# Optimization experiments

Measured on AMD Instinct MI355X. Metric: run time of the kernel, lower is better.

## Reference

```python
import jax, jax.numpy as jnp
import numpy as np

DR = 0.1
L = 24.0
N_FRAMES = 16
N_ATOMS = 512


def setup_inputs() -> dict:
    key = jax.random.key(0)
    # coordinates uniform in the periodic box [0, L)^3
    traj = jax.random.uniform(key, (N_FRAMES, N_ATOMS, 3), dtype=jnp.float32) * L
    cell = jnp.eye(3, dtype=jnp.float32) * L
    # r_list = arange(0.5*dr, L_max - 2*dr, dr) with L_max = cell[0,0]/2 -> 118 bins
    r_list = jnp.arange(0.5 * DR, L / 2 - 2 * DR, DR, dtype=jnp.float32)
    return {"traj": traj, "cell": cell, "r_list": r_list}


def _frame_hist(q, cell_diag, r_list, cutoff_sq):
    # q: [N,3]; dense minimum-image pairwise displacements, upper-triangle pairs only
    disp = q[None, :, :] - q[:, None, :]                        # [N,N,3]
    offsets = jax.lax.stop_gradient(jnp.floor(disp / cell_diag + 0.5))
    disp = disp - offsets * cell_diag                           # minimum image
    sq = jnp.sum(disp * disp, axis=-1)                          # [N,N]
    n = q.shape[0]
    triu = jnp.triu(jnp.ones((n, n), dtype=bool))               # torch.triu zeros lower part
    sq = jnp.where(triu, sq, 0.0)
    mask = (sq < cutoff_sq) & (sq != 0.0)                       # i<j and within cutoff
    d = jnp.sqrt(jnp.where(mask, sq, 1.0))                      # safe sqrt (masked out below)
    centered = d[:, :, None] - r_list[None, None, :]            # [N,N,B]
    g = (1.0 / (DR * np.sqrt(2.0 * np.pi))) * jnp.exp(-0.5 * (centered / DR) ** 2)
    g = g * mask[:, :, None].astype(g.dtype)                    # drop excluded pairs (== nonzero extraction)
    return g.sum(axis=(0, 1)) * DR                              # [B]


def reference(traj, cell, r_list):
    cell_diag = jnp.diag(cell)                                  # [3]
    cutoff_sq = (cell[0, 0] / 2.0) ** 2                         # L_max = cell[0,0]/2 (default)

    def step(acc, q):
        return acc + _frame_hist(q, cell_diag, r_list, cutoff_sq), None

    hist0 = jnp.zeros(r_list.shape, dtype=traj.dtype)
    hist, _ = jax.lax.scan(step, hist0, traj)                   # accumulate over frames like the python loop
    hist = hist / traj.shape[0]

    v = (4.0 * np.pi / 3.0) * ((r_list + 0.5 * DR) ** 3 - (r_list - 0.5 * DR) ** 3)
    natom = traj.shape[1]
    det = jnp.linalg.det(cell)
    gr = hist / v * det / (natom - 1) / natom * 2.0
    return (r_list, gr)
```

## Files before the change

kernel.cpp:

```cpp
#include <hip/hip_runtime.h>
#include <math.h>

#define N_ATOMS 512
#define MAX_B 128
#define NBUCK 128
#define WIN 0.40f

__global__ void zero_kernel(float* p, int n) {
    int t = blockIdx.x * blockDim.x + threadIdx.x;
    if (t < n) p[t] = 0.0f;
}

__global__ __launch_bounds__(256) void pair_kernel(
    const float* __restrict__ traj, const float* __restrict__ cell,
    const float* __restrict__ r_list, float* __restrict__ part,
    int B, int atomic_mode)
{
    __shared__ float2 qxy[N_ATOMS];
    __shared__ float  qzs[N_ATOMS];
    __shared__ float  dsorted[2048];
    __shared__ int    cnt[NBUCK];
    __shared__ int    start[NBUCK + 1];
    __shared__ int    cursor[NBUCK];
    __shared__ float  accbuf[256];

    const int frame = blockIdx.x >> 6;
    const int sub   = blockIdx.x & 63;
    const int tid   = threadIdx.x;

    const float* q = traj + (size_t)frame * (N_ATOMS * 3);
    for (int a = tid; a < N_ATOMS; a += 256) {
        qxy[a] = make_float2(q[3 * a + 0], q[3 * a + 1]);
        qzs[a] = q[3 * a + 2];
    }
    if (tid < NBUCK) cnt[tid] = 0;
    __syncthreads();

    const float L = cell[0];
    const float invL = 1.0f / L;
    const float cutoff_sq = 0.25f * L * L;
    const float inv_bw = (float)NBUCK / (0.5f * L);

    float dval[8];
    int   dbuck[8];
    #pragma unroll
    for (int s = 0; s < 8; ++s) {
        const int qidx = s * 256 + tid;
        const int rp   = sub * 4 + (qidx >> 9);
        const int qq   = qidx & 511;
        const int lenA = 511 - rp;
        const bool inA = qq < lenA;
        const int i = inA ? rp : (510 - rp);
        const int j = inA ? (rp + 1 + qq) : qq;
        const bool vp = !(rp == 255 && !inA);

        const float2 pj = qxy[j];
        const float2 pi = qxy[i];
        float dx = pj.x - pi.x;
        float dy = pj.y - pi.y;
        float dz = qzs[j] - qzs[i];
        dx -= L * floorf(dx * invL + 0.5f);
        dy -= L * floorf(dy * invL + 0.5f);
        dz -= L * floorf(dz * invL + 0.5f);
        const float d2 = dx * dx + dy * dy + dz * dz;

        dbuck[s] = -1;
        dval[s]  = 0.0f;
        if (vp && d2 < cutoff_sq && d2 != 0.0f) {
            const float d = sqrtf(d2);
            int b = (int)(d * inv_bw);
            if (b > NBUCK - 1) b = NBUCK - 1;
            dval[s]  = d;
            dbuck[s] = b;
            atomicAdd(&cnt[b], 1);
        }
    }
    __syncthreads();

    if (tid < 64) {
        const int c0 = cnt[2 * tid];
        const int c1 = cnt[2 * tid + 1];
        const int p  = c0 + c1;
        int incl = p;
        #pragma unroll
        for (int off = 1; off < 64; off <<= 1) {
            const int n = __shfl_up(incl, off, 64);
            if (tid >= off) incl += n;
        }
        start[2 * tid + 2]  = incl;
        start[2 * tid + 1]  = incl - c1;
        cursor[2 * tid]     = incl - p;
        cursor[2 * tid + 1] = incl - c1;
        if (tid == 0) start[0] = 0;
    }
    __syncthreads();

    #pragma unroll
    for (int s = 0; s < 8; ++s) {
        if (dbuck[s] >= 0) {
            const int pos = atomicAdd(&cursor[dbuck[s]], 1);
            dsorted[pos] = dval[s];
        }
    }
    __syncthreads();

    const int rot = (sub & 3) << 5;
    const int k = (tid + rot) & 127;
    const int g = tid >> 7;
    float acc = 0.0f;
    if (k < B) {
        const float rk = r_list[k];
        const float c1 = -50.0f;
        const float c2 = 100.0f * rk;
        const float c3 = -50.0f * rk * rk;
        int blo = (int)(fmaxf((rk - WIN) * inv_bw, 0.0f));
        int bhi = (int)((rk + WIN) * inv_bw);
        if (bhi > NBUCK - 1) bhi = NBUCK - 1;
        const int lo = start[blo];
        const int hi = start[bhi + 1];
        int idx = lo + g;
        int nn = hi - idx;
        nn = (nn > 0) ? ((nn + 1) >> 1) : 0;
        float acc1 = 0.0f;
        int m = nn >> 1;
        while (m-- > 0) {
            const float d0 = dsorted[idx];
            const float d1 = dsorted[idx + 2];
            idx += 4;
            acc  += __expf(fmaf(d0, fmaf(c1, d0, c2), c3));
            acc1 += __expf(fmaf(d1, fmaf(c1, d1, c2), c3));
        }
        if (nn & 1) {
            const float d0 = dsorted[idx];
            acc += __expf(fmaf(d0, fmaf(c1, d0, c2), c3));
        }
        acc += acc1;
    }
    accbuf[tid] = acc;
    __syncthreads();

    if (tid < 128) {
        const int kb = (tid + rot) & 127;
        const float v = accbuf[tid] + accbuf[tid + 128];
        if (atomic_mode) atomicAdd(&part[(blockIdx.x & 15) * MAX_B + kb], v);
        else             part[(size_t)blockIdx.x * MAX_B + kb] = v;
    }
}

__global__ __launch_bounds__(256) void finalize_kernel(
    const float* __restrict__ r_list, const float* __restrict__ cell,
    const float* __restrict__ part, float* __restrict__ out,
    int B, int F, int nrows)
{
    __shared__ float red[256];
    const int k = blockIdx.x;
    if (k >= B) return;

    float s = 0.0f;
    for (int t = threadIdx.x; t < nrows; t += 256) s += part[(size_t)t * MAX_B + k];
    red[threadIdx.x] = s;
    __syncthreads();
    for (int off = 128; off > 0; off >>= 1) {
        if (threadIdx.x < off) red[threadIdx.x] += red[threadIdx.x + off];
        __syncthreads();
    }
    if (threadIdx.x == 0) {
        const float r = r_list[k];
        out[k] = r;
        const float det = cell[0] * cell[4] * cell[8];
        const float rp = r + 0.05f;
        const float rm = r - 0.05f;
        const float v = (4.0f * (float)M_PI / 3.0f) * (rp * rp * rp - rm * rm * rm);
        const float inv_sqrt2pi = 0.3989422804014327f;
        const float h = red[0] * inv_sqrt2pi / (float)F;
        const float gr = h / v * det / (float)(N_ATOMS - 1) / (float)N_ATOMS * 2.0f;
        out[B + k] = gr;
    }
}

extern "C" void kernel_launch(void* const* d_in, const int* in_sizes, int n_in,
                              void* d_out, int out_size, void* d_ws, size_t ws_size,
                              hipStream_t stream) {
    const float* traj   = (const float*)d_in[0];
    const float* cell   = (const float*)d_in[1];
    const float* r_list = (const float*)d_in[2];
    float* out  = (float*)d_out;
    float* part = (float*)d_ws;

    const int B = in_sizes[2];
    const int F = in_sizes[0] / (N_ATOMS * 3);
    const int nblocks = F * 64;

    const bool partials_fit =
        ws_size >= (size_t)nblocks * MAX_B * sizeof(float);

    if (partials_fit) {
        hipLaunchKernelGGL(pair_kernel, dim3(nblocks), dim3(256), 0, stream,
                           traj, cell, r_list, part, B, 0);
        hipLaunchKernelGGL(finalize_kernel, dim3(MAX_B), dim3(256), 0, stream,
                           r_list, cell, part, out, B, F, nblocks);
    } else {
        hipLaunchKernelGGL(zero_kernel, dim3(8), dim3(256), 0, stream,
                           part, 16 * MAX_B);
        hipLaunchKernelGGL(pair_kernel, dim3(nblocks), dim3(256), 0, stream,
                           traj, cell, r_list, part, B, 1);
        hipLaunchKernelGGL(finalize_kernel, dim3(MAX_B), dim3(256), 0, stream,
                           r_list, cell, part, out, B, F, 16);
    }
}
```

Before: 69.44 us.

## Fuse finalize into pair kernel via last-block ticket and finer buckets

Replaces the separate finalize kernel with a last-block-done pattern: each block atomically adds its partial histogram into 16 replicated rows, takes a ticket, and the final block reduces the rows and writes the normalized output. The old zero kernel becomes a memset, so a whole kernel launch is dropped. The distance bucketing is also refined from 128 to 256 buckets and the Gaussian window narrowed from 0.40 to 0.35, so each bin visits fewer sorted distances. In exchange, global atomics contend across 1024 blocks and a device-wide fence is added. The narrower window slightly increases truncation of the Gaussian tail.

```diff
diff --git a/kernel.cpp b/kernel.cpp
--- a/kernel.cpp
+++ b/kernel.cpp
@@ -3,18 +3,15 @@
 
 #define N_ATOMS 512
 #define MAX_B 128
-#define NBUCK 128
-#define WIN 0.40f
-
-__global__ void zero_kernel(float* p, int n) {
-    int t = blockIdx.x * blockDim.x + threadIdx.x;
-    if (t < n) p[t] = 0.0f;
-}
+#define NBUCK 256
+#define NREP 16
+#define WIN 0.35f
 
 __global__ __launch_bounds__(256) void pair_kernel(
     const float* __restrict__ traj, const float* __restrict__ cell,
     const float* __restrict__ r_list, float* __restrict__ part,
-    int B, int atomic_mode)
+    unsigned int* __restrict__ ticket, float* __restrict__ out,
+    int B, int F, int nblocks)
 {
     __shared__ float2 qxy[N_ATOMS];
     __shared__ float  qzs[N_ATOMS];
@@ -78,19 +75,26 @@
     __syncthreads();
 
     if (tid < 64) {
-        const int c0 = cnt[2 * tid];
-        const int c1 = cnt[2 * tid + 1];
-        const int p  = c0 + c1;
+        const int c0 = cnt[4 * tid + 0];
+        const int c1 = cnt[4 * tid + 1];
+        const int c2 = cnt[4 * tid + 2];
+        const int c3 = cnt[4 * tid + 3];
+        const int p  = c0 + c1 + c2 + c3;
         int incl = p;
         #pragma unroll
         for (int off = 1; off < 64; off <<= 1) {
             const int n = __shfl_up(incl, off, 64);
             if (tid >= off) incl += n;
         }
-        start[2 * tid + 2]  = incl;
-        start[2 * tid + 1]  = incl - c1;
-        cursor[2 * tid]     = incl - p;
-        cursor[2 * tid + 1] = incl - c1;
+        const int base = incl - p;
+        start[4 * tid + 1] = base + c0;
+        start[4 * tid + 2] = base + c0 + c1;
+        start[4 * tid + 3] = base + c0 + c1 + c2;
+        start[4 * tid + 4] = incl;
+        cursor[4 * tid + 0] = base;
+        cursor[4 * tid + 1] = base + c0;
+        cursor[4 * tid + 2] = base + c0 + c1;
+        cursor[4 * tid + 3] = base + c0 + c1 + c2;
         if (tid == 0) start[0] = 0;
     }
     __syncthreads();
@@ -142,39 +146,34 @@
     if (tid < 128) {
         const int kb = (tid + rot) & 127;
         const float v = accbuf[tid] + accbuf[tid + 128];
-        if (atomic_mode) atomicAdd(&part[(blockIdx.x & 15) * MAX_B + kb], v);
-        else             part[(size_t)blockIdx.x * MAX_B + kb] = v;
+        atomicAdd(&part[(blockIdx.x & (NREP - 1)) * MAX_B + kb], v);
     }
-}
+    __threadfence();
+    __syncthreads();
 
-__global__ __launch_bounds__(256) void finalize_kernel(
-    const float* __restrict__ r_list, const float* __restrict__ cell,
-    const float* __restrict__ part, float* __restrict__ out,
-    int B, int F, int nrows)
-{
-    __shared__ float red[256];
-    const int k = blockIdx.x;
-    if (k >= B) return;
+    __shared__ unsigned int myticket;
+    if (tid == 0)
+        myticket = __hip_atomic_fetch_add(ticket, 1u, __ATOMIC_ACQ_REL,
+                                          __HIP_MEMORY_SCOPE_AGENT);
+    __syncthreads();
+    if (myticket != (unsigned int)(nblocks - 1)) return;
 
-    float s = 0.0f;
-    for (int t = threadIdx.x; t < nrows; t += 256) s += part[(size_t)t * MAX_B + k];
-    red[threadIdx.x] = s;
-    __syncthreads();
-    for (int off = 128; off > 0; off >>= 1) {
-        if (threadIdx.x < off) red[threadIdx.x] += red[threadIdx.x + off];
-        __syncthreads();
-    }
-    if (threadIdx.x == 0) {
-        const float r = r_list[k];
-        out[k] = r;
+    if (tid < MAX_B && tid < B) {
+        float s = 0.0f;
+        #pragma unroll
+        for (int ch = 0; ch < NREP; ++ch)
+            s += __hip_atomic_load(&part[ch * MAX_B + tid], __ATOMIC_RELAXED,
+                                   __HIP_MEMORY_SCOPE_AGENT);
+        const float r = r_list[tid];
+        out[tid] = r;
         const float det = cell[0] * cell[4] * cell[8];
         const float rp = r + 0.05f;
         const float rm = r - 0.05f;
         const float v = (4.0f * (float)M_PI / 3.0f) * (rp * rp * rp - rm * rm * rm);
         const float inv_sqrt2pi = 0.3989422804014327f;
-        const float h = red[0] * inv_sqrt2pi / (float)F;
+        const float h = s * inv_sqrt2pi / (float)F;
         const float gr = h / v * det / (float)(N_ATOMS - 1) / (float)N_ATOMS * 2.0f;
-        out[B + k] = gr;
+        out[B + tid] = gr;
     }
 }
 
@@ -186,25 +185,14 @@
     const float* r_list = (const float*)d_in[2];
     float* out  = (float*)d_out;
     float* part = (float*)d_ws;
+    unsigned int* ticket = (unsigned int*)(part + NREP * MAX_B);
 
     const int B = in_sizes[2];
     const int F = in_sizes[0] / (N_ATOMS * 3);
     const int nblocks = F * 64;
 
-    const bool partials_fit =
-        ws_size >= (size_t)nblocks * MAX_B * sizeof(float);
-
-    if (partials_fit) {
-        hipLaunchKernelGGL(pair_kernel, dim3(nblocks), dim3(256), 0, stream,
-                           traj, cell, r_list, part, B, 0);
-        hipLaunchKernelGGL(finalize_kernel, dim3(MAX_B), dim3(256), 0, stream,
-                           r_list, cell, part, out, B, F, nblocks);
-    } else {
-        hipLaunchKernelGGL(zero_kernel, dim3(8), dim3(256), 0, stream,
-                           part, 16 * MAX_B);
-        hipLaunchKernelGGL(pair_kernel, dim3(nblocks), dim3(256), 0, stream,
-                           traj, cell, r_list, part, B, 1);
-        hipLaunchKernelGGL(finalize_kernel, dim3(MAX_B), dim3(256), 0, stream,
-                           r_list, cell, part, out, B, F, 16);
-    }
+    hipMemsetAsync(part, 0, (size_t)(NREP * MAX_B) * sizeof(float) + sizeof(unsigned int),
+                   stream);
+    hipLaunchKernelGGL(pair_kernel, dim3(nblocks), dim3(256), 0, stream,
+                       traj, cell, r_list, part, ticket, out, B, F, nblocks);
 }
```

Result: slower. 139.0 us (+100.2%).
